# Kernel optimization log

Measured on AMD Instinct MI355X. Metric: run time of the kernel, lower is better.

## Reference

```python
import jax, jax.numpy as jnp
import numpy as np

N = 100000      # nodes
E = 1600000     # edges
R = 4           # relations
F = 128         # node feature dim
EMB = 128       # embedding size
HID = 256       # hidden size
B = 1024        # number of (nest, food) queries


def setup_inputs() -> dict:
    key = jax.random.key(0)
    ks = jax.random.split(key, 12)
    s1 = 1.0 / np.sqrt(F)
    s2 = 1.0 / np.sqrt(EMB)
    sf = 1.0 / np.sqrt(2 * EMB)
    return {
        "x": jax.random.normal(ks[0], (N, F), jnp.float32),
        "edge_index": jax.random.randint(ks[1], (2, E), 0, N),
        "edge_type": jax.random.randint(ks[2], (E,), 0, R),
        "nest_idx": jax.random.randint(ks[3], (B,), 0, N),
        "food_idx": jax.random.randint(ks[4], (B,), 0, N),
        "W_rel1": jax.random.normal(ks[5], (R, F, EMB), jnp.float32) * s1,
        "W_root1": jax.random.normal(ks[6], (F, EMB), jnp.float32) * s1,
        "b1": jnp.zeros((EMB,), jnp.float32),
        "W_rel2": jax.random.normal(ks[7], (R, EMB, EMB), jnp.float32) * s2,
        "W_root2": jax.random.normal(ks[8], (EMB, EMB), jnp.float32) * s2,
        "b2": jnp.zeros((EMB,), jnp.float32),
        "W_fc": jax.random.normal(ks[9], (2 * EMB, HID), jnp.float32) * sf,
        "b_fc": jnp.zeros((HID,), jnp.float32),
    }


def rgcn_conv(x, src, dst, etype, W_rel, W_root, b):
    # Per-relation transform of all nodes: [N, R, O]
    h = jnp.einsum('nf,rfo->nro', x, W_rel)
    msgs = h[src, etype]                      # [E, O] gather per edge
    # Mean aggregation per (dst, relation), PyG RGCNConv default
    key = dst * R + etype                     # [E]
    deg = jax.ops.segment_sum(jnp.ones((E,), x.dtype), key, num_segments=N * R)
    norm = 1.0 / jnp.maximum(deg, 1.0)
    out = jax.ops.segment_sum(msgs * norm[key][:, None], dst, num_segments=N)
    return out + x @ W_root + b


def reference(x, edge_index, edge_type, nest_idx, food_idx,
              W_rel1, W_root1, b1, W_rel2, W_root2, b2, W_fc, b_fc):
    src, dst = edge_index[0], edge_index[1]
    h = jax.nn.relu(rgcn_conv(x, src, dst, edge_type, W_rel1, W_root1, b1))
    h = rgcn_conv(h, src, dst, edge_type, W_rel2, W_root2, b2)
    combined = jnp.concatenate([h[nest_idx], h[food_idx]], axis=-1)  # [B, 2*EMB]
    return jax.nn.relu(combined @ W_fc + b_fc)                        # [B, HID]
```

## Files before the change

### kernel.cpp

```cpp
#include <hip/hip_runtime.h>
#include <stdint.h>

#define NN 100000
#define NE 1600000
#define NR 4
#define NK (NN * NR)
#define FD 128
#define KA 512
#define KT 640
#define NQ 1024
#define HIDN 256

#define NB 391
#define BSH 8
#define CAPB 8192
#define EPB 4096
#define NBLK1 ((NE + EPB - 1) / EPB)
#define MPAD 100096

using u16 = unsigned short;
using u32 = unsigned int;
typedef __attribute__((ext_vector_type(8))) __bf16 bf16x8;
typedef __attribute__((ext_vector_type(4))) float f32x4;

__device__ __forceinline__ u16 f2b(float f) {
    u32 u = __builtin_bit_cast(u32, f);
    u32 r = u + 0x7FFFu + ((u >> 16) & 1u);
    return (u16)(r >> 16);
}
__device__ __forceinline__ float b2f_lo(u32 v) { return __builtin_bit_cast(float, v << 16); }
__device__ __forceinline__ u32 pack2(float a, float b) {
    return (u32)f2b(a) | ((u32)f2b(b) << 16);
}
__device__ __forceinline__ void gload_lds16(const void* g, void* l) {
    __builtin_amdgcn_global_load_lds((const __attribute__((address_space(1))) u32*)g,
                                     (__attribute__((address_space(3))) u32*)l, 16, 0, 0);
}

__global__ __launch_bounds__(256) void bucket_scatter(const int* __restrict__ ei,
                                                      const int* __restrict__ et,
                                                      int* __restrict__ bcnt,
                                                      u32* __restrict__ bpack) {
    __shared__ int hist[NB];
    __shared__ int base[NB];
    int t = threadIdx.x;
    for (int i = t; i < NB; i += 256) hist[i] = 0;
    __syncthreads();
    int e0 = blockIdx.x * EPB;
    int rank[16];
    u32 pk[16];
    int bk[16];
#pragma unroll
    for (int j = 0; j < 16; ++j) {
        int e = e0 + j * 256 + t;
        bk[j] = -1;
        if (e < NE) {
            int src = __builtin_nontemporal_load(ei + e);
            int dst = __builtin_nontemporal_load(ei + NE + e);
            int r   = __builtin_nontemporal_load(et + e);
            bk[j] = dst >> BSH;
            pk[j] = (u32)src | ((u32)r << 17) | ((u32)(dst & 255) << 19);
            rank[j] = atomicAdd(&hist[bk[j]], 1);
        }
    }
    __syncthreads();
    for (int i = t; i < NB; i += 256) {
        int h = hist[i];
        base[i] = h ? atomicAdd(&bcnt[i], h) : 0;
    }
    __syncthreads();
#pragma unroll
    for (int j = 0; j < 16; ++j)
        if (bk[j] >= 0) bpack[(size_t)bk[j] * CAPB + base[bk[j]] + rank[j]] = pk[j];
}

__global__ __launch_bounds__(256) void key_scatter(const int* __restrict__ bcnt,
                                                   const u32* __restrict__ bpack,
                                                   int* __restrict__ offs6,
                                                   int* __restrict__ spack) {
    __shared__ int hist[1024];
    __shared__ int sm[256];
    int b = blockIdx.x, t = threadIdx.x;
    int cnt = bcnt[b];
    const u32* seg = bpack + (size_t)b * CAPB;
#pragma unroll
    for (int j = 0; j < 4; ++j) hist[t + j * 256] = 0;
    __syncthreads();
    for (int i = t; i < cnt; i += 256) atomicAdd(&hist[seg[i] >> 17], 1);
    __syncthreads();
    int t4 = t * 4;
    int h0 = hist[t4], h1 = hist[t4 + 1], h2 = hist[t4 + 2], h3 = hist[t4 + 3];
    int s = h0 + h1 + h2 + h3;
    int sp = (s + 7) & ~7;
    sm[t] = sp;
    __syncthreads();
    for (int o2 = 1; o2 < 256; o2 <<= 1) {
        int n = (t >= o2) ? sm[t - o2] : 0;
        __syncthreads();
        sm[t] += n;
        __syncthreads();
    }
    int bas = b * CAPB + sm[t] - sp;
    int e0 = bas, e1 = e0 + h0, e2 = e1 + h1, e3 = e2 + h2, e4 = e3 + h3, eL = bas + sp;
    int node = (b << 8) + t;
    if (node < NN) {
        int* o = offs6 + (size_t)node * 6;
        o[0] = e0; o[1] = e1; o[2] = e2; o[3] = e3; o[4] = e4; o[5] = eL;
    }
    hist[t4] = e0; hist[t4 + 1] = e1; hist[t4 + 2] = e2; hist[t4 + 3] = e3;
    for (int i = e4; i < eL; ++i) spack[i] = NN;
    __syncthreads();
    for (int i = t; i < cnt; i += 256) {
        u32 pk = seg[i];
        int pos = atomicAdd(&hist[pk >> 17], 1);
        spack[pos] = (int)(pk & 0x1FFFFu);
    }
}

__global__ __launch_bounds__(256) void cvt_bf16(const float* __restrict__ in,
                                                u16* __restrict__ outp, int n) {
    int i = blockIdx.x * 256 + threadIdx.x;
    int idx = i * 4;
    if (idx + 3 >= n) {
        for (int j = idx; j < n; ++j) outp[j] = f2b(in[j]);
        return;
    }
    float4 v = *(const float4*)(in + idx);
    u32 lo = (u32)f2b(v.x) | ((u32)f2b(v.y) << 16);
    u32 hi = (u32)f2b(v.z) | ((u32)f2b(v.w) << 16);
    *(uint2*)(outp + idx) = make_uint2(lo, hi);
}

__global__ __launch_bounds__(256) void prep_B(const float* __restrict__ Wrel,
                                              const float* __restrict__ Wroot,
                                              u16* __restrict__ Bt) {
    int i = blockIdx.x * 256 + threadIdx.x;
    if (i >= FD * KT) return;
    int k = i % KT;
    int o = i / KT;
    float v = (k < 512) ? Wrel[(size_t)k * FD + o] : Wroot[(size_t)(k - 512) * FD + o];
    Bt[i] = f2b(v);
}

__global__ __launch_bounds__(256) void agg_kernel(const int* __restrict__ offs6,
                                                  const int* __restrict__ spack,
                                                  const u32* __restrict__ fp,
                                                  u16* __restrict__ Aout,
                                                  int rows,
                                                  const int* __restrict__ nest,
                                                  const int* __restrict__ food,
                                                  int qmode,
                                                  int* __restrict__ qnodes) {
    int wid = threadIdx.x >> 6, lane = threadIdx.x & 63;
    int row = blockIdx.x * 4 + wid;
    if (row >= rows) return;
    int node;
    if (qmode) node = (row < NQ) ? nest[row] : food[row - NQ];
    else node = row;
    node = __builtin_amdgcn_readfirstlane(node);
    if (qmode && lane == 0) qnodes[row] = node;

    const int* ob = offs6 + (size_t)node * 6;
    int o0 = __builtin_amdgcn_readfirstlane(ob[0]);
    int o1 = __builtin_amdgcn_readfirstlane(ob[1]);
    int o2 = __builtin_amdgcn_readfirstlane(ob[2]);
    int o3 = __builtin_amdgcn_readfirstlane(ob[3]);
    int o4 = __builtin_amdgcn_readfirstlane(ob[4]);
    int oL = __builtin_amdgcn_readfirstlane(ob[5]);

    float a00 = 0, a01 = 0, a10 = 0, a11 = 0, a20 = 0, a21 = 0, a30 = 0, a31 = 0;

    for (int e = o0; e < oL; e += 8) {
        int p[8];
        u32 v[8];
#pragma unroll
        for (int j = 0; j < 8; ++j)
            p[j] = __builtin_amdgcn_readfirstlane(spack[e + j]);
#pragma unroll
        for (int j = 0; j < 8; ++j) v[j] = fp[(size_t)p[j] * 64 + lane];
#pragma unroll
        for (int j = 0; j < 8; ++j) {
            int ij = e + j;
            float f0 = b2f_lo(v[j]);
            float f1 = __builtin_bit_cast(float, v[j]);
            if (ij < o1)      { a00 += f0; a01 += f1; }
            else if (ij < o2) { a10 += f0; a11 += f1; }
            else if (ij < o3) { a20 += f0; a21 += f1; }
            else              { a30 += f0; a31 += f1; }
        }
    }

    int d0 = o1 - o0, d1 = o2 - o1, d2 = o3 - o2, d3 = o4 - o3;
    float s0 = 1.0f / (float)(d0 > 1 ? d0 : 1);
    float s1 = 1.0f / (float)(d1 > 1 ? d1 : 1);
    float s2 = 1.0f / (float)(d2 > 1 ? d2 : 1);
    float s3 = 1.0f / (float)(d3 > 1 ? d3 : 1);
    u16* Ao = Aout + (size_t)row * KA + lane * 2;
    __builtin_nontemporal_store(pack2(a00 * s0, a01 * s0), (u32*)(Ao + 0));
    __builtin_nontemporal_store(pack2(a10 * s1, a11 * s1), (u32*)(Ao + 128));
    __builtin_nontemporal_store(pack2(a20 * s2, a21 * s2), (u32*)(Ao + 256));
    __builtin_nontemporal_store(pack2(a30 * s3, a31 * s3), (u32*)(Ao + 384));
}

__global__ __launch_bounds__(256) void gemm_lds(const u16* __restrict__ A,
                                                const u16* __restrict__ rootSrc,
                                                const int* __restrict__ rootIdx,
                                                const u16* __restrict__ Bt,
                                                const float* __restrict__ bias,
                                                void* __restrict__ Cout,
                                                int M, int relu, int outBf16) {
    __shared__ u16 As[8192];
    char* lds = (char*)As;
    int tid = threadIdx.x;
    int wid = tid >> 6, lane = tid & 63;
    int wm = wid >> 1, wn = wid & 1;
    int lr = lane & 15, hi = lane >> 4;
    int row0 = blockIdx.x * 128;

    f32x4 acc[4][4];
#pragma unroll
    for (int i = 0; i < 4; ++i)
#pragma unroll
        for (int j = 0; j < 4; ++j) acc[i][j] = (f32x4){0.f, 0.f, 0.f, 0.f};

    int srow = wid * 8 + (lane >> 3);
    int sgl  = (lane & 7);

    for (int t = 0; t < 10; ++t) {
#pragma unroll
        for (int i = 0; i < 4; ++i) {
            int r = i * 32 + srow;
            int sg = sgl ^ (r & 7);
            int gr = row0 + r;
            const u16* src;
            if (t < 8) {
                src = A + (size_t)gr * KA + t * 64 + sg * 8;
            } else {
                int idx = rootIdx ? rootIdx[gr] : gr;
                src = rootSrc + (size_t)idx * FD + (t - 8) * 64 + sg * 8;
            }
            gload_lds16(src, lds + i * 4096 + wid * 1024);
        }
        bf16x8 bfr[2][4];
#pragma unroll
        for (int kk = 0; kk < 2; ++kk)
#pragma unroll
            for (int ni = 0; ni < 4; ++ni) {
                int col = wn * 64 + ni * 16 + lr;
                bfr[kk][ni] = *reinterpret_cast<const bf16x8*>(
                    Bt + (size_t)col * KT + t * 64 + kk * 32 + hi * 8);
            }
        __syncthreads();
#pragma unroll
        for (int kk = 0; kk < 2; ++kk) {
            bf16x8 afr[4];
#pragma unroll
            for (int mi = 0; mi < 4; ++mi) {
                int r = wm * 64 + mi * 16 + lr;
                int sp = (kk * 4 + hi) ^ (r & 7);
                afr[mi] = *reinterpret_cast<const bf16x8*>(lds + r * 128 + sp * 16);
            }
#pragma unroll
            for (int mi = 0; mi < 4; ++mi)
#pragma unroll
                for (int ni = 0; ni < 4; ++ni)
                    acc[mi][ni] = __builtin_amdgcn_mfma_f32_16x16x32_bf16(afr[mi], bfr[kk][ni], acc[mi][ni], 0, 0, 0);
        }
        __syncthreads();
    }

#pragma unroll
    for (int mi = 0; mi < 4; ++mi) {
#pragma unroll
        for (int ni = 0; ni < 4; ++ni) {
            int col = wn * 64 + ni * 16 + lr;
            float bv = bias[col];
#pragma unroll
            for (int rg = 0; rg < 4; ++rg) {
                int row = row0 + wm * 64 + mi * 16 + hi * 4 + rg;
                if (row < M) {
                    float v = acc[mi][ni][rg] + bv;
                    if (relu) v = fmaxf(v, 0.f);
                    if (outBf16) ((u16*)Cout)[(size_t)row * FD + col] = f2b(v);
                    else ((float*)Cout)[(size_t)row * FD + col] = v;
                }
            }
        }
    }
}

__global__ __launch_bounds__(256) void fc_kernel(const float* __restrict__ h2q,
                                                 const float* __restrict__ Wfc,
                                                 const float* __restrict__ bfc,
                                                 float* __restrict__ out) {
    __shared__ float comb[2 * FD];
    int q = blockIdx.x, t = threadIdx.x;
    if (t < FD) comb[t] = h2q[(size_t)q * FD + t];
    else comb[t] = h2q[(size_t)(NQ + q) * FD + (t - FD)];
    __syncthreads();
    float s = bfc[t];
#pragma unroll 4
    for (int k = 0; k < 2 * FD; ++k) s += comb[k] * Wfc[(size_t)k * HIDN + t];
    out[(size_t)q * HIDN + t] = fmaxf(s, 0.f);
}

extern "C" void kernel_launch(void* const* d_in, const int* in_sizes, int n_in,
                              void* d_out, int out_size, void* d_ws, size_t ws_size,
                              hipStream_t stream) {
    const float* x      = (const float*)d_in[0];
    const int*   ei     = (const int*)d_in[1];
    const int*   et     = (const int*)d_in[2];
    const int*   nest   = (const int*)d_in[3];
    const int*   food   = (const int*)d_in[4];
    const float* Wrel1  = (const float*)d_in[5];
    const float* Wroot1 = (const float*)d_in[6];
    const float* b1     = (const float*)d_in[7];
    const float* Wrel2  = (const float*)d_in[8];
    const float* Wroot2 = (const float*)d_in[9];
    const float* b2     = (const float*)d_in[10];
    const float* Wfc    = (const float*)d_in[11];
    const float* bfc    = (const float*)d_in[12];
    float* out = (float*)d_out;

    char* w = (char*)d_ws;
    size_t off = 0;
    auto take = [&](size_t b) {
        char* p = w + off;
        off += b;
        off = (off + 255) & ~(size_t)255;
        return p;
    };
    int* bcnt   = (int*)take((size_t)NB * 4);
    int* offs6  = (int*)take((size_t)NN * 6 * 4);
    u32* bpack  = (u32*)take((size_t)NB * CAPB * 4);
    int* spack  = (int*)take((size_t)NB * CAPB * 4);
    int* qnodes = (int*)take((size_t)2 * NQ * 4);
    u16* xh     = (u16*)take((size_t)MPAD * FD * 2);
    u16* h1     = (u16*)take((size_t)MPAD * FD * 2);
    u16* Bt1    = (u16*)take((size_t)FD * KT * 2);
    u16* Bt2    = (u16*)take((size_t)FD * KT * 2);
    u16* A1     = (u16*)take((size_t)MPAD * KA * 2);
    u16* A2     = (u16*)take((size_t)2 * NQ * KA * 2);
    float* h2q  = (float*)take((size_t)2 * NQ * FD * 4);

    hipMemsetAsync(bcnt, 0, (size_t)NB * 4, stream);
    hipMemsetAsync(xh + (size_t)NN * FD, 0, FD * 2, stream);
    hipMemsetAsync(h1 + (size_t)NN * FD, 0, FD * 2, stream);
    cvt_bf16<<<((NN * FD / 4) + 255) / 256, 256, 0, stream>>>(x, xh, NN * FD);
    prep_B<<<(FD * KT + 255) / 256, 256, 0, stream>>>(Wrel1, Wroot1, Bt1);
    prep_B<<<(FD * KT + 255) / 256, 256, 0, stream>>>(Wrel2, Wroot2, Bt2);
    bucket_scatter<<<NBLK1, 256, 0, stream>>>(ei, et, bcnt, bpack);
    key_scatter<<<NB, 256, 0, stream>>>(bcnt, bpack, offs6, spack);

    agg_kernel<<<(NN + 3) / 4, 256, 0, stream>>>(offs6, spack, (const u32*)xh, A1,
                                                 NN, nullptr, nullptr, 0, nullptr);
    gemm_lds<<<MPAD / 128, 256, 0, stream>>>(A1, xh, nullptr, Bt1, b1,
                                             (void*)h1, NN, 1, 1);

    agg_kernel<<<(2 * NQ + 3) / 4, 256, 0, stream>>>(offs6, spack, (const u32*)h1, A2,
                                                     2 * NQ, nest, food, 1, qnodes);
    gemm_lds<<<(2 * NQ) / 128, 256, 0, stream>>>(A2, h1, qnodes, Bt2, b2,
                                                 (void*)h2q, 2 * NQ, 0, 0);
    fc_kernel<<<NQ, 256, 0, stream>>>(h2q, Wfc, bfc, out);
}
```

Baseline: 257.6 us.

## Double-buffer GEMM LDS staging with 64-row tiles and fix bf16 high-half decode

The GEMM kernel now uses 64-row tiles, which doubles the number of blocks, and two LDS buffers. The next K-slice is loaded into one buffer while MFMA runs on the other, which overlaps global-to-LDS traffic with compute. The intent is to cut load stalls and improve occupancy on the large layer-1 GEMM. The aggregation kernel now masks off the low bits when decoding the high bf16 half, and the cvt tail path is simplified to assume n is a multiple of 4. The loop appears to keep the single trailing __syncthreads, so a block could overwrite a buffer before every wave has finished reading it, which is a race risk.

```diff
diff --git a/kernel.cpp b/kernel.cpp
--- a/kernel.cpp
+++ b/kernel.cpp
@@ -29,6 +29,7 @@
     return (u16)(r >> 16);
 }
 __device__ __forceinline__ float b2f_lo(u32 v) { return __builtin_bit_cast(float, v << 16); }
+__device__ __forceinline__ float b2f_hi(u32 v) { return __builtin_bit_cast(float, v & 0xFFFF0000u); }
 __device__ __forceinline__ u32 pack2(float a, float b) {
     return (u32)f2b(a) | ((u32)f2b(b) << 16);
 }
@@ -121,10 +122,7 @@
                                                 u16* __restrict__ outp, int n) {
     int i = blockIdx.x * 256 + threadIdx.x;
     int idx = i * 4;
-    if (idx + 3 >= n) {
-        for (int j = idx; j < n; ++j) outp[j] = f2b(in[j]);
-        return;
-    }
+    if (idx >= n) return;
     float4 v = *(const float4*)(in + idx);
     u32 lo = (u32)f2b(v.x) | ((u32)f2b(v.y) << 16);
     u32 hi = (u32)f2b(v.z) | ((u32)f2b(v.w) << 16);
@@ -182,7 +180,7 @@
         for (int j = 0; j < 8; ++j) {
             int ij = e + j;
             float f0 = b2f_lo(v[j]);
-            float f1 = __builtin_bit_cast(float, v[j]);
+            float f1 = b2f_hi(v[j]);
             if (ij < o1)      { a00 += f0; a01 += f1; }
             else if (ij < o2) { a10 += f0; a11 += f1; }
             else if (ij < o3) { a20 += f0; a21 += f1; }
@@ -202,35 +200,33 @@
     __builtin_nontemporal_store(pack2(a30 * s3, a31 * s3), (u32*)(Ao + 384));
 }
 
-__global__ __launch_bounds__(256) void gemm_lds(const u16* __restrict__ A,
-                                                const u16* __restrict__ rootSrc,
-                                                const int* __restrict__ rootIdx,
-                                                const u16* __restrict__ Bt,
-                                                const float* __restrict__ bias,
-                                                void* __restrict__ Cout,
-                                                int M, int relu, int outBf16) {
-    __shared__ u16 As[8192];
-    char* lds = (char*)As;
+__global__ __launch_bounds__(256) void gemm_lds64(const u16* __restrict__ A,
+                                                  const u16* __restrict__ rootSrc,
+                                                  const int* __restrict__ rootIdx,
+                                                  const u16* __restrict__ Bt,
+                                                  const float* __restrict__ bias,
+                                                  void* __restrict__ Cout,
+                                                  int M, int relu, int outBf16) {
+    __shared__ u16 As[2][4096];
     int tid = threadIdx.x;
     int wid = tid >> 6, lane = tid & 63;
     int wm = wid >> 1, wn = wid & 1;
     int lr = lane & 15, hi = lane >> 4;
-    int row0 = blockIdx.x * 128;
-
-    f32x4 acc[4][4];
-#pragma unroll
-    for (int i = 0; i < 4; ++i)
+    int row0 = blockIdx.x * 64;
+
+    f32x4 acc[2][4];
+#pragma unroll
+    for (int i = 0; i < 2; ++i)
 #pragma unroll
         for (int j = 0; j < 4; ++j) acc[i][j] = (f32x4){0.f, 0.f, 0.f, 0.f};
 
     int srow = wid * 8 + (lane >> 3);
-    int sgl  = (lane & 7);
-
-    for (int t = 0; t < 10; ++t) {
-#pragma unroll
-        for (int i = 0; i < 4; ++i) {
+    int sg = (lane & 7) ^ (lane >> 3);
+
+    auto stage = [&](int t, int buf) {
+#pragma unroll
+        for (int i = 0; i < 2; ++i) {
             int r = i * 32 + srow;
-            int sg = sgl ^ (r & 7);
             int gr = row0 + r;
             const u16* src;
             if (t < 8) {
@@ -239,8 +235,15 @@
                 int idx = rootIdx ? rootIdx[gr] : gr;
                 src = rootSrc + (size_t)idx * FD + (t - 8) * 64 + sg * 8;
             }
-            gload_lds16(src, lds + i * 4096 + wid * 1024);
-        }
+            gload_lds16(src, (char*)As[buf] + i * 4096 + wid * 1024);
+        }
+    };
+
+    stage(0, 0);
+    __syncthreads();
+
+    for (int t = 0; t < 10; ++t) {
+        int cur = t & 1;
         bf16x8 bfr[2][4];
 #pragma unroll
         for (int kk = 0; kk < 2; ++kk)
@@ -250,18 +253,18 @@
                 bfr[kk][ni] = *reinterpret_cast<const bf16x8*>(
                     Bt + (size_t)col * KT + t * 64 + kk * 32 + hi * 8);
             }
-        __syncthreads();
+        if (t + 1 < 10) stage(t + 1, cur ^ 1);
 #pragma unroll
         for (int kk = 0; kk < 2; ++kk) {
-            bf16x8 afr[4];
-#pragma unroll
-            for (int mi = 0; mi < 4; ++mi) {
-                int r = wm * 64 + mi * 16 + lr;
-                int sp = (kk * 4 + hi) ^ (r & 7);
-                afr[mi] = *reinterpret_cast<const bf16x8*>(lds + r * 128 + sp * 16);
+            bf16x8 afr[2];
+#pragma unroll
+            for (int mi = 0; mi < 2; ++mi) {
+                int r = wm * 32 + mi * 16 + lr;
+                int sp = (kk * 4 + hi) ^ (lr & 7);
+                afr[mi] = *reinterpret_cast<const bf16x8*>((char*)As[cur] + r * 128 + sp * 16);
             }
 #pragma unroll
-            for (int mi = 0; mi < 4; ++mi)
+            for (int mi = 0; mi < 2; ++mi)
 #pragma unroll
                 for (int ni = 0; ni < 4; ++ni)
                     acc[mi][ni] = __builtin_amdgcn_mfma_f32_16x16x32_bf16(afr[mi], bfr[kk][ni], acc[mi][ni], 0, 0, 0);
@@ -270,14 +273,14 @@
     }
 
 #pragma unroll
-    for (int mi = 0; mi < 4; ++mi) {
+    for (int mi = 0; mi < 2; ++mi) {
 #pragma unroll
         for (int ni = 0; ni < 4; ++ni) {
             int col = wn * 64 + ni * 16 + lr;
             float bv = bias[col];
 #pragma unroll
             for (int rg = 0; rg < 4; ++rg) {
-                int row = row0 + wm * 64 + mi * 16 + hi * 4 + rg;
+                int row = row0 + wm * 32 + mi * 16 + hi * 4 + rg;
                 if (row < M) {
                     float v = acc[mi][ni][rg] + bv;
                     if (relu) v = fmaxf(v, 0.f);
@@ -354,12 +357,12 @@
 
     agg_kernel<<<(NN + 3) / 4, 256, 0, stream>>>(offs6, spack, (const u32*)xh, A1,
                                                  NN, nullptr, nullptr, 0, nullptr);
-    gemm_lds<<<MPAD / 128, 256, 0, stream>>>(A1, xh, nullptr, Bt1, b1,
-                                             (void*)h1, NN, 1, 1);
+    gemm_lds64<<<MPAD / 64, 256, 0, stream>>>(A1, xh, nullptr, Bt1, b1,
+                                              (void*)h1, NN, 1, 1);
 
     agg_kernel<<<(2 * NQ + 3) / 4, 256, 0, stream>>>(offs6, spack, (const u32*)h1, A2,
                                                      2 * NQ, nest, food, 1, qnodes);
-    gemm_lds<<<(2 * NQ) / 128, 256, 0, stream>>>(A2, h1, qnodes, Bt2, b2,
-                                                 (void*)h2q, 2 * NQ, 0, 0);
+    gemm_lds64<<<(2 * NQ) / 64, 256, 0, stream>>>(A2, h1, qnodes, Bt2, b2,
+                                                  (void*)h2q, 2 * NQ, 0, 0);
     fc_kernel<<<NQ, 256, 0, stream>>>(h2q, Wfc, bfc, out);
 }
```

After: 272.6 us. 5.8% more time.

## Triple-buffer GEMM LDS staging with async global-to-LDS prefetch two steps ahead

Applied to the files above, without the earlier changes.

Replaces the single-buffer LDS GEMM with a three-buffer version that issues the global-to-LDS loads for K-step t+2 while computing step t. It waits with explicit vmcnt counts instead of full __syncthreads, which should hide load latency behind MFMA work. The cost is three times the LDS per block, which can lower occupancy. It also masks the low half when unpacking the high bf16 in aggregation and simplifies the tail handling in cvt_bf16.

```diff
diff --git a/kernel.cpp b/kernel.cpp
--- a/kernel.cpp
+++ b/kernel.cpp
@@ -29,6 +29,7 @@
     return (u16)(r >> 16);
 }
 __device__ __forceinline__ float b2f_lo(u32 v) { return __builtin_bit_cast(float, v << 16); }
+__device__ __forceinline__ float b2f_hi(u32 v) { return __builtin_bit_cast(float, v & 0xFFFF0000u); }
 __device__ __forceinline__ u32 pack2(float a, float b) {
     return (u32)f2b(a) | ((u32)f2b(b) << 16);
 }
@@ -121,10 +122,7 @@
                                                 u16* __restrict__ outp, int n) {
     int i = blockIdx.x * 256 + threadIdx.x;
     int idx = i * 4;
-    if (idx + 3 >= n) {
-        for (int j = idx; j < n; ++j) outp[j] = f2b(in[j]);
-        return;
-    }
+    if (idx >= n) return;
     float4 v = *(const float4*)(in + idx);
     u32 lo = (u32)f2b(v.x) | ((u32)f2b(v.y) << 16);
     u32 hi = (u32)f2b(v.z) | ((u32)f2b(v.w) << 16);
@@ -182,7 +180,7 @@
         for (int j = 0; j < 8; ++j) {
             int ij = e + j;
             float f0 = b2f_lo(v[j]);
-            float f1 = __builtin_bit_cast(float, v[j]);
+            float f1 = b2f_hi(v[j]);
             if (ij < o1)      { a00 += f0; a01 += f1; }
             else if (ij < o2) { a10 += f0; a11 += f1; }
             else if (ij < o3) { a20 += f0; a21 += f1; }
@@ -202,15 +200,14 @@
     __builtin_nontemporal_store(pack2(a30 * s3, a31 * s3), (u32*)(Ao + 384));
 }
 
-__global__ __launch_bounds__(256) void gemm_lds(const u16* __restrict__ A,
-                                                const u16* __restrict__ rootSrc,
-                                                const int* __restrict__ rootIdx,
-                                                const u16* __restrict__ Bt,
-                                                const float* __restrict__ bias,
-                                                void* __restrict__ Cout,
-                                                int M, int relu, int outBf16) {
-    __shared__ u16 As[8192];
-    char* lds = (char*)As;
+__global__ __launch_bounds__(256) void gemm_lds3(const u16* __restrict__ A,
+                                                 const u16* __restrict__ rootSrc,
+                                                 const int* __restrict__ rootIdx,
+                                                 const u16* __restrict__ Bt,
+                                                 const float* __restrict__ bias,
+                                                 void* __restrict__ Cout,
+                                                 int M, int relu, int outBf16) {
+    __shared__ u16 As[3][8192];
     int tid = threadIdx.x;
     int wid = tid >> 6, lane = tid & 63;
     int wm = wid >> 1, wn = wid & 1;
@@ -224,13 +221,12 @@
         for (int j = 0; j < 4; ++j) acc[i][j] = (f32x4){0.f, 0.f, 0.f, 0.f};
 
     int srow = wid * 8 + (lane >> 3);
-    int sgl  = (lane & 7);
-
-    for (int t = 0; t < 10; ++t) {
+    int sg = (lane & 7) ^ ((lane >> 3) & 7);
+
+    auto stage = [&](int t, int buf) {
 #pragma unroll
         for (int i = 0; i < 4; ++i) {
             int r = i * 32 + srow;
-            int sg = sgl ^ (r & 7);
             int gr = row0 + r;
             const u16* src;
             if (t < 8) {
@@ -239,8 +235,15 @@
                 int idx = rootIdx ? rootIdx[gr] : gr;
                 src = rootSrc + (size_t)idx * FD + (t - 8) * 64 + sg * 8;
             }
-            gload_lds16(src, lds + i * 4096 + wid * 1024);
-        }
+            gload_lds16(src, (char*)As[buf] + i * 4096 + wid * 1024);
+        }
+    };
+
+    stage(0, 0);
+    stage(1, 1);
+
+    for (int t = 0; t < 10; ++t) {
+        int cur = t % 3;
         bf16x8 bfr[2][4];
 #pragma unroll
         for (int kk = 0; kk < 2; ++kk)
@@ -250,7 +253,12 @@
                 bfr[kk][ni] = *reinterpret_cast<const bf16x8*>(
                     Bt + (size_t)col * KT + t * 64 + kk * 32 + hi * 8);
             }
-        __syncthreads();
+        bool staged = (t + 2 < 10);
+        if (staged) stage(t + 2, (t + 2) % 3);
+        if (staged) asm volatile("s_waitcnt vmcnt(4)" ::: "memory");
+        else        asm volatile("s_waitcnt vmcnt(0)" ::: "memory");
+        __builtin_amdgcn_s_barrier();
+        __builtin_amdgcn_sched_barrier(0);
 #pragma unroll
         for (int kk = 0; kk < 2; ++kk) {
             bf16x8 afr[4];
@@ -258,7 +266,7 @@
             for (int mi = 0; mi < 4; ++mi) {
                 int r = wm * 64 + mi * 16 + lr;
                 int sp = (kk * 4 + hi) ^ (r & 7);
-                afr[mi] = *reinterpret_cast<const bf16x8*>(lds + r * 128 + sp * 16);
+                afr[mi] = *reinterpret_cast<const bf16x8*>((char*)As[cur] + r * 128 + sp * 16);
             }
 #pragma unroll
             for (int mi = 0; mi < 4; ++mi)
@@ -266,7 +274,8 @@
                 for (int ni = 0; ni < 4; ++ni)
                     acc[mi][ni] = __builtin_amdgcn_mfma_f32_16x16x32_bf16(afr[mi], bfr[kk][ni], acc[mi][ni], 0, 0, 0);
         }
-        __syncthreads();
+        asm volatile("s_waitcnt lgkmcnt(0)" ::: "memory");
+        __builtin_amdgcn_s_barrier();
     }
 
 #pragma unroll
@@ -354,12 +363,12 @@
 
     agg_kernel<<<(NN + 3) / 4, 256, 0, stream>>>(offs6, spack, (const u32*)xh, A1,
                                                  NN, nullptr, nullptr, 0, nullptr);
-    gemm_lds<<<MPAD / 128, 256, 0, stream>>>(A1, xh, nullptr, Bt1, b1,
-                                             (void*)h1, NN, 1, 1);
+    gemm_lds3<<<MPAD / 128, 256, 0, stream>>>(A1, xh, nullptr, Bt1, b1,
+                                              (void*)h1, NN, 1, 1);
 
     agg_kernel<<<(2 * NQ + 3) / 4, 256, 0, stream>>>(offs6, spack, (const u32*)h1, A2,
                                                      2 * NQ, nest, food, 1, qnodes);
-    gemm_lds<<<(2 * NQ) / 128, 256, 0, stream>>>(A2, h1, qnodes, Bt2, b2,
-                                                 (void*)h2q, 2 * NQ, 0, 0);
+    gemm_lds3<<<(2 * NQ) / 128, 256, 0, stream>>>(A2, h1, qnodes, Bt2, b2,
+                                                  (void*)h2q, 2 * NQ, 0, 0);
     fc_kernel<<<NQ, 256, 0, stream>>>(h2q, Wfc, bfc, out);
 }
```

After: 259.8 us. About the same (+0.9%).
